# Kernel optimization log

Measured on AMD Instinct MI355X. Metric: run time of the kernel, lower is better.

The kernel has to match this reference:

```python
import jax, jax.numpy as jnp
import numpy as np

NUM_LAYERS = 8
HIDDEN = 128
BATCH = 262144
SKIP_CONNECTION = True
BIAS_ENABLED = True


def setup_inputs() -> dict:
    key = jax.random.key(0)
    kx, kw, kb = jax.random.split(key, 3)
    x = jax.random.normal(kx, (BATCH, HIDDEN), dtype=jnp.float32)
    # scale weights ~ 1/sqrt(fan_in) so activations stay O(1) across 8 layers
    w = jax.random.normal(kw, (NUM_LAYERS, HIDDEN, HIDDEN), dtype=jnp.float32) * (1.0 / np.sqrt(HIDDEN))
    b = jax.random.normal(kb, (NUM_LAYERS, HIDDEN), dtype=jnp.float32) * 0.01
    return {"x": x, "w": w, "b": b}


def reference(x, w, b):
    # Fused elastic MLP, full-width (active_neurons == hidden for every layer).
    # Per the Triton forward kernel: every layer (including the last) applies
    # ReLU, and with skip_connection the input block is added AFTER the
    # activation for layers > 0.
    h = x
    for layer in range(NUM_LAYERS):
        h = jax.nn.relu(jnp.einsum('bi,ji->bj', h, w[layer]) + (b[layer] if BIAS_ENABLED else 0.0))
        if SKIP_CONNECTION and layer > 0:
            h = h + x  # input_dim == hidden, skip-add over full width
    return h
```

## Files before the change

### kernel.cpp

```cpp
#include <hip/hip_runtime.h>
#include <hip/hip_bf16.h>


typedef __bf16 bf16_t;
typedef __bf16 bf16x8 __attribute__((ext_vector_type(8)));
typedef __bf16 bf16x4 __attribute__((ext_vector_type(4)));
typedef float floatx4 __attribute__((ext_vector_type(4)));

#define HID 128
#define NLAYERS 8
#define TM 128
#define LDH 136

__global__ __launch_bounds__(256) void wconv_kernel(const float* __restrict__ w,
                                                    bf16_t* __restrict__ wb) {
    int i = (blockIdx.x * 256 + threadIdx.x) * 4;
    floatx4 v = *(const floatx4*)&w[i];
    bf16x4 o = { (bf16_t)v[0], (bf16_t)v[1], (bf16_t)v[2], (bf16_t)v[3] };
    *(bf16x4*)&wb[i] = o;
}

__global__ __launch_bounds__(256, 2) void mlp_kernel(
    const float* __restrict__ x, const bf16_t* __restrict__ wb,
    const float* __restrict__ bias, float* __restrict__ out)
{
    __shared__ __align__(16) bf16_t hs[TM][LDH];
    __shared__ __align__(16) bf16_t wsh[HID][LDH];

    const int tid  = threadIdx.x;
    const int wave = tid >> 6;
    const int lane = tid & 63;
    const int c16  = lane & 15;
    const int quad = lane >> 4;
    const int m0 = (wave >> 1) * 64;
    const int n0 = (wave & 1) * 64;
    const long rowbase = (long)blockIdx.x * TM;
    const int jb = m0 + quad * 4;

    floatx4 xr[4][4];
#pragma unroll
    for (int ni = 0; ni < 4; ++ni) {
        const float* xrow = x + (rowbase + n0 + ni*16 + c16) * HID;
#pragma unroll
        for (int mi = 0; mi < 4; ++mi)
            xr[mi][ni] = *(const floatx4*)&xrow[jb + mi*16];
    }
#pragma unroll
    for (int ni = 0; ni < 4; ++ni) {
        bf16_t* hrow = &hs[n0 + ni*16 + c16][0];
#pragma unroll
        for (int mi = 0; mi < 4; ++mi) {
            floatx4 v = xr[mi][ni];
            bf16x4 o = { (bf16_t)v[0], (bf16_t)v[1], (bf16_t)v[2], (bf16_t)v[3] };
            *(bf16x4*)&hrow[jb + mi*16] = o;
        }
    }

    const bf16x8* wbv = (const bf16x8*)wb;
    bf16x8 wreg[8];
#pragma unroll
    for (int p = 0; p < 8; ++p) wreg[p] = wbv[p*256 + tid];
    floatx4 bnext[4];
#pragma unroll
    for (int mi = 0; mi < 4; ++mi) bnext[mi] = *(const floatx4*)&bias[jb + mi*16];

    for (int l = 0; l < NLAYERS; ++l) {
#pragma unroll
        for (int p = 0; p < 8; ++p) {
            int f = p*256 + tid;
            *(bf16x8*)&wsh[f >> 4][(f & 15) * 8] = wreg[p];
        }
        __syncthreads();

        floatx4 acc[4][4];
#pragma unroll
        for (int mi = 0; mi < 4; ++mi)
#pragma unroll
          for (int ni = 0; ni < 4; ++ni)
            acc[mi][ni] = bnext[mi];

        if (l + 1 < NLAYERS) {
#pragma unroll
            for (int p = 0; p < 8; ++p) wreg[p] = wbv[(l+1)*2048 + p*256 + tid];
#pragma unroll
            for (int mi = 0; mi < 4; ++mi)
                bnext[mi] = *(const floatx4*)&bias[(l+1)*HID + jb + mi*16];
        }

#pragma unroll
        for (int k = 0; k < 4; ++k) {
            const int kc = k*32 + quad*8;
            bf16x8 af[4], bf[4];
#pragma unroll
            for (int mi = 0; mi < 4; ++mi)
                af[mi] = *(const bf16x8*)&wsh[m0 + mi*16 + c16][kc];
#pragma unroll
            for (int ni = 0; ni < 4; ++ni)
                bf[ni] = *(const bf16x8*)&hs[n0 + ni*16 + c16][kc];
#pragma unroll
            for (int mi = 0; mi < 4; ++mi)
#pragma unroll
              for (int ni = 0; ni < 4; ++ni)
                acc[mi][ni] = __builtin_amdgcn_mfma_f32_16x16x32_bf16(
                                  af[mi], bf[ni], acc[mi][ni], 0, 0, 0);
        }
        __syncthreads();

        if (l < NLAYERS - 1) {
#pragma unroll
            for (int ni = 0; ni < 4; ++ni) {
                bf16_t* hrow = &hs[n0 + ni*16 + c16][0];
#pragma unroll
                for (int mi = 0; mi < 4; ++mi) {
                    floatx4 v = acc[mi][ni];
                    float s0 = fmaxf(v[0], 0.0f), s1 = fmaxf(v[1], 0.0f);
                    float s2 = fmaxf(v[2], 0.0f), s3 = fmaxf(v[3], 0.0f);
                    if (l > 0) {
                        floatx4 xv = xr[mi][ni];
                        s0 += xv[0]; s1 += xv[1]; s2 += xv[2]; s3 += xv[3];
                    }
                    bf16x4 o = { (bf16_t)s0, (bf16_t)s1, (bf16_t)s2, (bf16_t)s3 };
                    *(bf16x4*)&hrow[jb + mi*16] = o;
                }
            }
        } else {
#pragma unroll
            for (int ni = 0; ni < 4; ++ni) {
                float* orow = out + (rowbase + n0 + ni*16 + c16) * HID;
#pragma unroll
                for (int mi = 0; mi < 4; ++mi) {
                    floatx4 v = acc[mi][ni];
                    floatx4 xv = xr[mi][ni];
                    floatx4 o;
                    o[0] = fmaxf(v[0], 0.0f) + xv[0];
                    o[1] = fmaxf(v[1], 0.0f) + xv[1];
                    o[2] = fmaxf(v[2], 0.0f) + xv[2];
                    o[3] = fmaxf(v[3], 0.0f) + xv[3];
                    *(floatx4*)&orow[jb + mi*16] = o;
                }
            }
        }
    }
}

extern "C" void kernel_launch(void* const* d_in, const int* in_sizes, int n_in,
                              void* d_out, int out_size, void* d_ws, size_t ws_size,
                              hipStream_t stream) {
    const float* x = (const float*)d_in[0];
    const float* w = (const float*)d_in[1];
    const float* b = (const float*)d_in[2];
    float* out = (float*)d_out;
    bf16_t* wb = (bf16_t*)d_ws;

    wconv_kernel<<<NLAYERS*HID*HID/(256*4), 256, 0, stream>>>(w, wb);

    const int nblocks = 262144 / TM;
    mlp_kernel<<<nblocks, 256, 0, stream>>>(x, wb, b, out);
}
```

Before: 286.4 us.

## Load weight fragments directly to registers and double-buffer activation LDS

Weight MFMA fragments are now read directly from global memory (L2-resident bf16) into registers, which removes the weight LDS staging buffer and its per-layer store and barrier. The activation tile is double-buffered in LDS, so each layer needs only one barrier instead of two. Next-layer weight fragments are prefetched per k-step right after that step's MFMAs. The trade-off is higher register pressure (64 VGPRs held for af) and more scattered global loads in place of coalesced ones.

```diff
diff --git a/kernel.cpp b/kernel.cpp
--- a/kernel.cpp
+++ b/kernel.cpp
@@ -24,8 +24,7 @@
     const float* __restrict__ x, const bf16_t* __restrict__ wb,
     const float* __restrict__ bias, float* __restrict__ out)
 {
-    __shared__ __align__(16) bf16_t hs[TM][LDH];
-    __shared__ __align__(16) bf16_t wsh[HID][LDH];
+    __shared__ __align__(16) bf16_t hs[2][TM][LDH];
 
     const int tid  = threadIdx.x;
     const int wave = tid >> 6;
@@ -47,7 +46,7 @@
     }
 #pragma unroll
     for (int ni = 0; ni < 4; ++ni) {
-        bf16_t* hrow = &hs[n0 + ni*16 + c16][0];
+        bf16_t* hrow = &hs[0][n0 + ni*16 + c16][0];
 #pragma unroll
         for (int mi = 0; mi < 4; ++mi) {
             floatx4 v = xr[mi][ni];
@@ -56,21 +55,24 @@
         }
     }
 
-    const bf16x8* wbv = (const bf16x8*)wb;
-    bf16x8 wreg[8];
+    const bf16_t* wl = wb + (m0 + c16) * HID + quad * 8;
+
+    bf16x8 af[4][4];
 #pragma unroll
-    for (int p = 0; p < 8; ++p) wreg[p] = wbv[p*256 + tid];
+    for (int mi = 0; mi < 4; ++mi)
+#pragma unroll
+      for (int k = 0; k < 4; ++k)
+        af[mi][k] = *(const bf16x8*)&wl[mi*16*HID + k*32];
+
     floatx4 bnext[4];
 #pragma unroll
     for (int mi = 0; mi < 4; ++mi) bnext[mi] = *(const floatx4*)&bias[jb + mi*16];
 
+    __syncthreads();
+
+#pragma unroll
     for (int l = 0; l < NLAYERS; ++l) {
-#pragma unroll
-        for (int p = 0; p < 8; ++p) {
-            int f = p*256 + tid;
-            *(bf16x8*)&wsh[f >> 4][(f & 15) * 8] = wreg[p];
-        }
-        __syncthreads();
+        const int cur = l & 1;
 
         floatx4 acc[4][4];
 #pragma unroll
@@ -81,35 +83,35 @@
 
         if (l + 1 < NLAYERS) {
 #pragma unroll
-            for (int p = 0; p < 8; ++p) wreg[p] = wbv[(l+1)*2048 + p*256 + tid];
-#pragma unroll
             for (int mi = 0; mi < 4; ++mi)
                 bnext[mi] = *(const floatx4*)&bias[(l+1)*HID + jb + mi*16];
         }
 
+        const bf16_t* wnext = wl + (l + 1) * HID * HID;
 #pragma unroll
         for (int k = 0; k < 4; ++k) {
             const int kc = k*32 + quad*8;
-            bf16x8 af[4], bf[4];
-#pragma unroll
-            for (int mi = 0; mi < 4; ++mi)
-                af[mi] = *(const bf16x8*)&wsh[m0 + mi*16 + c16][kc];
+            bf16x8 bfr[4];
 #pragma unroll
             for (int ni = 0; ni < 4; ++ni)
-                bf[ni] = *(const bf16x8*)&hs[n0 + ni*16 + c16][kc];
+                bfr[ni] = *(const bf16x8*)&hs[cur][n0 + ni*16 + c16][kc];
 #pragma unroll
             for (int mi = 0; mi < 4; ++mi)
 #pragma unroll
               for (int ni = 0; ni < 4; ++ni)
                 acc[mi][ni] = __builtin_amdgcn_mfma_f32_16x16x32_bf16(
-                                  af[mi], bf[ni], acc[mi][ni], 0, 0, 0);
+                                  af[mi][k], bfr[ni], acc[mi][ni], 0, 0, 0);
+            if (l + 1 < NLAYERS) {
+#pragma unroll
+                for (int mi = 0; mi < 4; ++mi)
+                    af[mi][k] = *(const bf16x8*)&wnext[mi*16*HID + k*32];
+            }
         }
-        __syncthreads();
 
         if (l < NLAYERS - 1) {
 #pragma unroll
             for (int ni = 0; ni < 4; ++ni) {
-                bf16_t* hrow = &hs[n0 + ni*16 + c16][0];
+                bf16_t* hrow = &hs[cur ^ 1][n0 + ni*16 + c16][0];
 #pragma unroll
                 for (int mi = 0; mi < 4; ++mi) {
                     floatx4 v = acc[mi][ni];
@@ -123,6 +125,7 @@
                     *(bf16x4*)&hrow[jb + mi*16] = o;
                 }
             }
+            __syncthreads();
         } else {
 #pragma unroll
             for (int ni = 0; ni < 4; ++ni) {
```

Result: slower. 331.6 us (+15.8%).

## Keep activations in registers with 32x32 MFMA and permlane swaps, drop LDS

Applied to the files above, without the earlier changes.

Each wave now owns 32 batch rows and computes all 128 outputs with 32x32x16 bf16 MFMAs. The layer output is repacked into the next layer's B-operand entirely in registers using v_permlane32_swap, so the shared-memory staging of activations and weights, and the block-wide barriers, are gone. Weights are pre-swizzled into MFMA fragment order by the conversion kernel and streamed from global/L2 per layer, with a two-deep register prefetch. This removes the LDS traffic and syncs, but every wave now re-reads the full weight matrix from cache and register pressure rises.

```diff
diff --git a/kernel.cpp b/kernel.cpp
--- a/kernel.cpp
+++ b/kernel.cpp
@@ -4,141 +4,133 @@
 
 typedef __bf16 bf16_t;
 typedef __bf16 bf16x8 __attribute__((ext_vector_type(8)));
-typedef __bf16 bf16x4 __attribute__((ext_vector_type(4)));
 typedef float floatx4 __attribute__((ext_vector_type(4)));
+typedef float floatx16 __attribute__((ext_vector_type(16)));
+typedef unsigned int uintx4 __attribute__((ext_vector_type(4)));
 
 #define HID 128
 #define NLAYERS 8
-#define TM 128
-#define LDH 136
+
+static __device__ __forceinline__ unsigned pk(float a, float b) {
+    union { bf16_t h[2]; unsigned u; } r;
+    r.h[0] = (bf16_t)a; r.h[1] = (bf16_t)b;
+    return r.u;
+}
+static __device__ __forceinline__ void plswap(unsigned& a, unsigned& b) {
+    asm volatile("v_permlane32_swap_b32 %0, %1" : "+v"(a), "+v"(b));
+}
 
 __global__ __launch_bounds__(256) void wconv_kernel(const float* __restrict__ w,
                                                     bf16_t* __restrict__ wb) {
-    int i = (blockIdx.x * 256 + threadIdx.x) * 4;
-    floatx4 v = *(const floatx4*)&w[i];
-    bf16x4 o = { (bf16_t)v[0], (bf16_t)v[1], (bf16_t)v[2], (bf16_t)v[3] };
-    *(bf16x4*)&wb[i] = o;
+    int t = blockIdx.x * 256 + threadIdx.x;
+    int lane = t & 63, kk = (t >> 6) & 7, mi = (t >> 9) & 3, l = t >> 11;
+    int row = 32*mi + (lane & 31);
+    int col = 16*kk + 8*(lane >> 5);
+    const float* src = w + ((l*HID + row)*HID + col);
+    floatx4 v0 = *(const floatx4*)src;
+    floatx4 v1 = *(const floatx4*)(src + 4);
+    bf16x8 o = { (bf16_t)v0[0], (bf16_t)v0[1], (bf16_t)v0[2], (bf16_t)v0[3],
+                 (bf16_t)v1[0], (bf16_t)v1[1], (bf16_t)v1[2], (bf16_t)v1[3] };
+    *(bf16x8*)(wb + (long)t * 8) = o;
 }
 
 __global__ __launch_bounds__(256, 2) void mlp_kernel(
     const float* __restrict__ x, const bf16_t* __restrict__ wb,
     const float* __restrict__ bias, float* __restrict__ out)
 {
-    __shared__ __align__(16) bf16_t hs[TM][LDH];
-    __shared__ __align__(16) bf16_t wsh[HID][LDH];
-
     const int tid  = threadIdx.x;
-    const int wave = tid >> 6;
     const int lane = tid & 63;
-    const int c16  = lane & 15;
-    const int quad = lane >> 4;
-    const int m0 = (wave >> 1) * 64;
-    const int n0 = (wave & 1) * 64;
-    const long rowbase = (long)blockIdx.x * TM;
-    const int jb = m0 + quad * 4;
+    const int col  = lane & 31;
+    const int hi4  = (lane >> 5) * 4;
+    const long row = (long)blockIdx.x * 128 + (tid >> 6) * 32 + col;
+    const float* xrow = x + row * HID;
 
     floatx4 xr[4][4];
 #pragma unroll
-    for (int ni = 0; ni < 4; ++ni) {
-        const float* xrow = x + (rowbase + n0 + ni*16 + c16) * HID;
+    for (int mi = 0; mi < 4; ++mi)
 #pragma unroll
-        for (int mi = 0; mi < 4; ++mi)
-            xr[mi][ni] = *(const floatx4*)&xrow[jb + mi*16];
-    }
+      for (int g = 0; g < 4; ++g)
+        xr[mi][g] = *(const floatx4*)&xrow[32*mi + 8*g + hi4];
+
+    bf16x8 hf[8];
 #pragma unroll
-    for (int ni = 0; ni < 4; ++ni) {
-        bf16_t* hrow = &hs[n0 + ni*16 + c16][0];
-#pragma unroll
-        for (int mi = 0; mi < 4; ++mi) {
-            floatx4 v = xr[mi][ni];
-            bf16x4 o = { (bf16_t)v[0], (bf16_t)v[1], (bf16_t)v[2], (bf16_t)v[3] };
-            *(bf16x4*)&hrow[jb + mi*16] = o;
-        }
+    for (int kk = 0; kk < 8; ++kk) {
+        const int mi = kk >> 1, h2 = (kk & 1) * 2;
+        floatx4 A = xr[mi][h2], B = xr[mi][h2 + 1];
+        unsigned pa0 = pk(A[0], A[1]), pa1 = pk(A[2], A[3]);
+        unsigned pb0 = pk(B[0], B[1]), pb1 = pk(B[2], B[3]);
+        plswap(pa0, pb0); plswap(pa1, pb1);
+        uintx4 u = { pa0, pa1, pb0, pb1 };
+        hf[kk] = __builtin_bit_cast(bf16x8, u);
     }
 
     const bf16x8* wbv = (const bf16x8*)wb;
-    bf16x8 wreg[8];
-#pragma unroll
-    for (int p = 0; p < 8; ++p) wreg[p] = wbv[p*256 + tid];
-    floatx4 bnext[4];
-#pragma unroll
-    for (int mi = 0; mi < 4; ++mi) bnext[mi] = *(const floatx4*)&bias[jb + mi*16];
 
     for (int l = 0; l < NLAYERS; ++l) {
-#pragma unroll
-        for (int p = 0; p < 8; ++p) {
-            int f = p*256 + tid;
-            *(bf16x8*)&wsh[f >> 4][(f & 15) * 8] = wreg[p];
-        }
-        __syncthreads();
-
-        floatx4 acc[4][4];
+        floatx16 acc[4];
 #pragma unroll
         for (int mi = 0; mi < 4; ++mi)
 #pragma unroll
-          for (int ni = 0; ni < 4; ++ni)
-            acc[mi][ni] = bnext[mi];
+          for (int g = 0; g < 4; ++g) {
+            floatx4 bv = *(const floatx4*)&bias[l*HID + 32*mi + 8*g + hi4];
+            acc[mi][4*g+0] = bv[0]; acc[mi][4*g+1] = bv[1];
+            acc[mi][4*g+2] = bv[2]; acc[mi][4*g+3] = bv[3];
+          }
 
-        if (l + 1 < NLAYERS) {
+        const long lbase = (long)l * 32;
+        bf16x8 af0[4], af1[4];
 #pragma unroll
-            for (int p = 0; p < 8; ++p) wreg[p] = wbv[(l+1)*2048 + p*256 + tid];
+        for (int mi = 0; mi < 4; ++mi) af0[mi] = wbv[(lbase + mi*8 + 0)*64 + lane];
+#pragma unroll
+        for (int mi = 0; mi < 4; ++mi) af1[mi] = wbv[(lbase + mi*8 + 1)*64 + lane];
+#pragma unroll
+        for (int kk = 0; kk < 8; ++kk) {
+            bf16x8 acur[4];
+#pragma unroll
+            for (int mi = 0; mi < 4; ++mi) acur[mi] = (kk & 1) ? af1[mi] : af0[mi];
+            if (kk + 2 < 8) {
+#pragma unroll
+                for (int mi = 0; mi < 4; ++mi) {
+                    bf16x8 v = wbv[(lbase + mi*8 + kk + 2)*64 + lane];
+                    if (kk & 1) af1[mi] = v; else af0[mi] = v;
+                }
+            }
 #pragma unroll
             for (int mi = 0; mi < 4; ++mi)
-                bnext[mi] = *(const floatx4*)&bias[(l+1)*HID + jb + mi*16];
+                acc[mi] = __builtin_amdgcn_mfma_f32_32x32x16_bf16(
+                              acur[mi], hf[kk], acc[mi], 0, 0, 0);
         }
 
+        if (l < NLAYERS - 1) {
 #pragma unroll
-        for (int k = 0; k < 4; ++k) {
-            const int kc = k*32 + quad*8;
-            bf16x8 af[4], bf[4];
+            for (int kk = 0; kk < 8; ++kk) {
+                const int mi = kk >> 1, hh = kk & 1;
+                float s[8];
 #pragma unroll
-            for (int mi = 0; mi < 4; ++mi)
-                af[mi] = *(const bf16x8*)&wsh[m0 + mi*16 + c16][kc];
-#pragma unroll
-            for (int ni = 0; ni < 4; ++ni)
-                bf[ni] = *(const bf16x8*)&hs[n0 + ni*16 + c16][kc];
+                for (int j = 0; j < 4; ++j) {
+                    float va = fmaxf(acc[mi][8*hh + j],     0.0f);
+                    float vb = fmaxf(acc[mi][8*hh + 4 + j], 0.0f);
+                    if (l > 0) { va += xr[mi][2*hh][j]; vb += xr[mi][2*hh+1][j]; }
+                    s[j] = va; s[4 + j] = vb;
+                }
+                unsigned pa0 = pk(s[0], s[1]), pa1 = pk(s[2], s[3]);
+                unsigned pb0 = pk(s[4], s[5]), pb1 = pk(s[6], s[7]);
+                plswap(pa0, pb0); plswap(pa1, pb1);
+                uintx4 u = { pa0, pa1, pb0, pb1 };
+                hf[kk] = __builtin_bit_cast(bf16x8, u);
+            }
+        } else {
+            float* orow = out + row * HID;
 #pragma unroll
             for (int mi = 0; mi < 4; ++mi)
 #pragma unroll
-              for (int ni = 0; ni < 4; ++ni)
-                acc[mi][ni] = __builtin_amdgcn_mfma_f32_16x16x32_bf16(
-                                  af[mi], bf[ni], acc[mi][ni], 0, 0, 0);
-        }
-        __syncthreads();
-
-        if (l < NLAYERS - 1) {
+              for (int g = 0; g < 4; ++g) {
+                floatx4 o;
 #pragma unroll
-            for (int ni = 0; ni < 4; ++ni) {
-                bf16_t* hrow = &hs[n0 + ni*16 + c16][0];
-#pragma unroll
-                for (int mi = 0; mi < 4; ++mi) {
-                    floatx4 v = acc[mi][ni];
-                    float s0 = fmaxf(v[0], 0.0f), s1 = fmaxf(v[1], 0.0f);
-                    float s2 = fmaxf(v[2], 0.0f), s3 = fmaxf(v[3], 0.0f);
-                    if (l > 0) {
-                        floatx4 xv = xr[mi][ni];
-                        s0 += xv[0]; s1 += xv[1]; s2 += xv[2]; s3 += xv[3];
-                    }
-                    bf16x4 o = { (bf16_t)s0, (bf16_t)s1, (bf16_t)s2, (bf16_t)s3 };
-                    *(bf16x4*)&hrow[jb + mi*16] = o;
-                }
-            }
-        } else {
-#pragma unroll
-            for (int ni = 0; ni < 4; ++ni) {
-                float* orow = out + (rowbase + n0 + ni*16 + c16) * HID;
-#pragma unroll
-                for (int mi = 0; mi < 4; ++mi) {
-                    floatx4 v = acc[mi][ni];
-                    floatx4 xv = xr[mi][ni];
-                    floatx4 o;
-                    o[0] = fmaxf(v[0], 0.0f) + xv[0];
-                    o[1] = fmaxf(v[1], 0.0f) + xv[1];
-                    o[2] = fmaxf(v[2], 0.0f) + xv[2];
-                    o[3] = fmaxf(v[3], 0.0f) + xv[3];
-                    *(floatx4*)&orow[jb + mi*16] = o;
-                }
-            }
+                for (int j = 0; j < 4; ++j)
+                    o[j] = fmaxf(acc[mi][4*g + j], 0.0f) + xr[mi][g][j];
+                *(floatx4*)&orow[32*mi + 8*g + hi4] = o;
+              }
         }
     }
 }
@@ -152,8 +144,8 @@
     float* out = (float*)d_out;
     bf16_t* wb = (bf16_t*)d_ws;
 
-    wconv_kernel<<<NLAYERS*HID*HID/(256*4), 256, 0, stream>>>(w, wb);
+    wconv_kernel<<<NLAYERS*HID*HID/(256*8), 256, 0, stream>>>(w, wb);
 
-    const int nblocks = 262144 / TM;
+    const int nblocks = 262144 / 128;
     mlp_kernel<<<nblocks, 256, 0, stream>>>(x, wb, b, out);
 }
```

After: 341.7 us. 1.19x slower.
